# Performance work log

Measured on AMD Instinct MI355X. Metric: run time of the kernel, lower is better.

Reference implementation:

```python
import jax, jax.numpy as jnp
import numpy as np

N = 50000
E = 800000
IN_C = 512
HID = 256
OUT_C = 2
NUM_LAYERS = 3
NUM_HIER = 3
EPS = 1e-5


def setup_inputs() -> dict:
    key = jax.random.key(0)
    ks = jax.random.split(key, 24)
    g = lambda k, shp, fan: jax.random.normal(k, shp, jnp.float32) / np.sqrt(fan)
    inp = {
        "x": jax.random.normal(ks[0], (N, IN_C), jnp.float32),
        "edge_index": jax.random.randint(ks[1], (2, E), 0, N, jnp.int64),
        # GCN conv weights/biases
        "conv_w0": g(ks[2], (IN_C, HID), IN_C),
        "conv_ws": g(ks[3], (NUM_LAYERS - 1, HID, HID), HID),
        "conv_b": jnp.zeros((NUM_LAYERS, HID), jnp.float32),
        "bn_g": jnp.ones((NUM_LAYERS, HID), jnp.float32),
        "bn_b": jnp.zeros((NUM_LAYERS, HID), jnp.float32),
        # global-path MLPs
        "fcg_w0": g(ks[4], (HID, HID), HID),
        "fcg_ws": g(ks[5], (NUM_HIER - 1, 2 * HID, HID), 2 * HID),
        "fcg_b": jnp.zeros((NUM_HIER, HID), jnp.float32),
        "bng_g": jnp.ones((NUM_HIER, HID), jnp.float32),
        "bng_b": jnp.zeros((NUM_HIER, HID), jnp.float32),
        # local-path MLPs
        "fcl_w": g(ks[6], (NUM_HIER, HID, HID), HID),
        "fcl_b": jnp.zeros((NUM_HIER, HID), jnp.float32),
        "bnl_g": jnp.ones((NUM_HIER, HID), jnp.float32),
        "bnl_b": jnp.zeros((NUM_HIER, HID), jnp.float32),
        # output heads
        "outg_w": g(ks[7], (HID, OUT_C), HID),
        "outg_b": jnp.zeros((OUT_C,), jnp.float32),
        "outl_w": g(ks[8], (NUM_HIER, HID, OUT_C), HID),
        "outl_b": jnp.zeros((NUM_HIER, OUT_C), jnp.float32),
    }
    return inp


def _gcn_edges(edge_index):
    # add self-loops, compute symmetric normalization D^-1/2 (A+I) D^-1/2
    loops = jnp.arange(N, dtype=edge_index.dtype)
    rows = jnp.concatenate([edge_index[0], loops])
    cols = jnp.concatenate([edge_index[1], loops])
    deg = jax.ops.segment_sum(jnp.ones_like(rows, jnp.float32), rows, num_segments=N)
    dinv = jnp.where(deg > 0, jax.lax.rsqrt(deg), 0.0)
    w = dinv[rows] * dinv[cols]
    return rows, cols, w


def _propagate(h, rows, cols, w):
    msg = h[cols] * w[:, None]          # [E+N, HID] gather
    return jax.ops.segment_sum(msg, rows, num_segments=N)


def _bn(h, gamma, beta):
    m = h.mean(0)
    v = h.var(0)
    return gamma * (h - m) * jax.lax.rsqrt(v + EPS) + beta


def reference(x, edge_index, conv_w0, conv_ws, conv_b, bn_g, bn_b,
              fcg_w0, fcg_ws, fcg_b, bng_g, bng_b,
              fcl_w, fcl_b, bnl_g, bnl_b,
              outg_w, outg_b, outl_w, outl_b):
    rows, cols, ew = _gcn_edges(edge_index)
    h = x
    for i in range(NUM_LAYERS):
        W = conv_w0 if i == 0 else conv_ws[i - 1]
        h = _propagate(h @ W, rows, cols, ew) + conv_b[i]
        h = jax.nn.relu(_bn(h, bn_g[i], bn_b[i]))  # dropout = identity (eval)
    # hierarchical global path
    hg = []
    xg = jax.nn.relu(_bn(h @ fcg_w0 + fcg_b[0], bng_g[0], bng_b[0]))
    hg.append(xg)
    for i in range(NUM_HIER - 1):
        xg = jnp.concatenate([hg[i], h], -1) @ fcg_ws[i] + fcg_b[i + 1]
        xg = jax.nn.relu(_bn(xg, bng_g[i + 1], bng_b[i + 1]))
        hg.append(xg)
    og = jax.nn.log_softmax(hg[-1] @ outg_w + outg_b, axis=-1)
    # local heads
    ol = []
    for i in range(NUM_HIER):
        hl = jax.nn.relu(_bn(hg[i] @ fcl_w[i] + fcl_b[i], bnl_g[i], bnl_b[i]))
        ol.append(jax.nn.log_softmax(hl @ outl_w[i] + outl_b[i], axis=-1))
    # stack: [1 + NUM_HIER, N, OUT_C] (og first, then local heads)
    return jnp.stack([og] + ol, axis=0)
```

## Files before the change

kernel.cpp:

```cpp
#include <hip/hip_runtime.h>
#include <math.h>

#define N_NODES 50000
#define E_EDGES 800000
#define HID 256
#define EPS_BN 1e-5f

#define AGG_BPS 256

typedef __attribute__((ext_vector_type(8))) short short8;
typedef __attribute__((ext_vector_type(4))) float floatx4;
typedef __attribute__((ext_vector_type(8))) unsigned short ushort8v;

__device__ __forceinline__ unsigned short f2bf(float f) {
    unsigned u = __float_as_uint(f);
    u = (u + 0x7FFFu + ((u >> 16) & 1u)) >> 16;
    return (unsigned short)u;
}
__device__ __forceinline__ float bf2f(unsigned short b) {
    return __uint_as_float(((unsigned)b) << 16);
}
__device__ __forceinline__ void bn_scsh(const float* stats, const float* gamma,
                                        const float* beta, int ch,
                                        float& sc, float& sh) {
    const float invn = 1.0f / (float)N_NODES;
    float mean = stats[ch] * invn;
    float var = stats[HID + ch] * invn - mean * mean;
    var = fmaxf(var, 0.f);
    sc = gamma[ch] * rsqrtf(var + EPS_BN);
    sh = beta[ch] - mean * sc;
}

__global__ __launch_bounds__(256) void k_deg(const int* __restrict__ rows,
                                             int* __restrict__ deg) {
    int e = blockIdx.x * 256 + threadIdx.x;
    atomicAdd(&deg[rows[e]], 1);
}

__global__ __launch_bounds__(256) void k_dinv(const int* __restrict__ deg,
                                              float* __restrict__ dinv) {
    int n = blockIdx.x * 256 + threadIdx.x;
    if (n < N_NODES) dinv[n] = rsqrtf((float)deg[n] + 1.0f);
}

__global__ __launch_bounds__(1024) void k_scan(const int* __restrict__ deg,
                                               int* __restrict__ rowptr) {
    __shared__ int wsum[16];
    __shared__ int carry_s;
    int tid = threadIdx.x, lane = tid & 63, w = tid >> 6;
    if (tid == 0) carry_s = 0;
    __syncthreads();
    for (int base = 0; base < N_NODES; base += 1024) {
        int v = (base + tid < N_NODES) ? deg[base + tid] : 0;
        int x = v;
#pragma unroll
        for (int d = 1; d < 64; d <<= 1) {
            int t = __shfl_up(x, d);
            if (lane >= d) x += t;
        }
        if (lane == 63) wsum[w] = x;
        __syncthreads();
        if (w == 0) {
            int ws = (lane < 16) ? wsum[lane] : 0;
#pragma unroll
            for (int d = 1; d < 16; d <<= 1) {
                int t = __shfl_up(ws, d);
                if (lane >= d) ws += t;
            }
            if (lane < 16) wsum[lane] = ws;
        }
        __syncthreads();
        int c = carry_s;
        int wbase = (w > 0) ? wsum[w - 1] : 0;
        if (base + tid < N_NODES) rowptr[base + tid] = c + wbase + x - v;
        __syncthreads();
        if (tid == 0) carry_s = c + wsum[15];
        __syncthreads();
    }
    if (threadIdx.x == 0) rowptr[N_NODES] = carry_s;
}

__global__ __launch_bounds__(256) void k_fill(const int* __restrict__ rows,
                                              const int* __restrict__ cols,
                                              const int* __restrict__ rowptr,
                                              int* __restrict__ cursor,
                                              int* __restrict__ colidx) {
    int e = blockIdx.x * 256 + threadIdx.x;
    int r = rows[e];
    int pos = atomicAdd(&cursor[r], 1);
    colidx[rowptr[r] + pos] = cols[e];
}

__global__ __launch_bounds__(256) void k_f2bf_slice(const float* __restrict__ X,
                                                    unsigned short* __restrict__ Y) {
    int i = blockIdx.x * 256 + threadIdx.x;
    int slice = i / (N_NODES * 4);
    int rem = i - slice * (N_NODES * 4);
    int node = rem >> 2, p8 = rem & 3;
    const float* xp = X + (size_t)node * 512 + slice * 32 + p8 * 8;
    float4 va = ((const float4*)xp)[0];
    float4 vb = ((const float4*)xp)[1];
    ushort8v o;
    o[0] = f2bf(va.x); o[1] = f2bf(va.y); o[2] = f2bf(va.z); o[3] = f2bf(va.w);
    o[4] = f2bf(vb.x); o[5] = f2bf(vb.y); o[6] = f2bf(vb.z); o[7] = f2bf(vb.w);
    *(ushort8v*)(Y + (size_t)i * 8) = o;
}

__global__ __launch_bounds__(256) void k_wt(const float* __restrict__ W,
                                            unsigned short* __restrict__ Wt,
                                            int K) {
    int idx = blockIdx.x * 256 + threadIdx.x;
    if (idx >= K * HID) return;
    int k = idx >> 8;
    int n = idx & (HID - 1);
    Wt[(size_t)n * K + k] = f2bf(W[idx]);
}

__global__ __launch_bounds__(256) void k_gemm_mfma(
    const unsigned short* __restrict__ A0,
    const unsigned short* __restrict__ A1, int K0, int K,
    const unsigned short* __restrict__ Bt,
    unsigned short* __restrict__ C,
    const float* __restrict__ rowscale,
    float* __restrict__ stats)
{
    __shared__ alignas(16) unsigned short As[128 * 32];
    __shared__ alignas(16) unsigned short Bs[128 * 32];
    int tid = threadIdx.x;
    int wid = tid >> 6, lane = tid & 63;
    int row0 = blockIdx.x * 128;
    int n0 = blockIdx.y * 128;
    int wrow = (wid & 1) * 64, wcol = (wid >> 1) * 64;
    int lr = lane >> 2;
    int lk = (lane & 3) * 8;
    int qq = lane >> 4, mr = lane & 15;

    floatx4 acc[4][4];
#pragma unroll
    for (int i = 0; i < 4; ++i)
#pragma unroll
        for (int j = 0; j < 4; ++j) {
            floatx4 z = {0.f, 0.f, 0.f, 0.f};
            acc[i][j] = z;
        }

    for (int k0 = 0; k0 < K; k0 += 32) {
        const unsigned short* Abase =
            (k0 < K0) ? A0 + (size_t)(k0 >> 5) * (N_NODES * 32)
                      : A1 + (size_t)((k0 - K0) >> 5) * (N_NODES * 32);
#pragma unroll
        for (int i = 0; i < 2; ++i) {
            int rloc = wid * 32 + i * 16 + lr;
            int grow = row0 + rloc;
            if (grow > N_NODES - 1) grow = N_NODES - 1;
            const unsigned short* g = Abase + (size_t)grow * 32 + lk;
            unsigned short* l = As + (wid * 32 + i * 16) * 32;
            __builtin_amdgcn_global_load_lds(
                (const __attribute__((address_space(1))) void*)g,
                (__attribute__((address_space(3))) void*)l, 16, 0, 0);
        }
#pragma unroll
        for (int i = 0; i < 2; ++i) {
            int nloc = wid * 32 + i * 16 + lr;
            const unsigned short* g = Bt + (size_t)(n0 + nloc) * K + k0 + lk;
            unsigned short* l = Bs + (wid * 32 + i * 16) * 32;
            __builtin_amdgcn_global_load_lds(
                (const __attribute__((address_space(1))) void*)g,
                (__attribute__((address_space(3))) void*)l, 16, 0, 0);
        }
        __syncthreads();
        short8 af[4], bfv[4];
#pragma unroll
        for (int i = 0; i < 4; ++i)
            af[i] = *(const short8*)(As + (wrow + i * 16 + mr) * 32 + qq * 8);
#pragma unroll
        for (int j = 0; j < 4; ++j)
            bfv[j] = *(const short8*)(Bs + (wcol + j * 16 + mr) * 32 + qq * 8);
#pragma unroll
        for (int i = 0; i < 4; ++i)
#pragma unroll
            for (int j = 0; j < 4; ++j)
                acc[i][j] = __builtin_amdgcn_mfma_f32_16x16x32_bf16(
                    af[i], bfv[j], acc[i][j], 0, 0, 0);
        __syncthreads();
    }

    float* ls = (float*)As;
    float* lq = ((float*)As) + 128;
    if (stats) {
        ((float*)As)[tid] = 0.f;
        __syncthreads();
    }

    float psum[4] = {0.f, 0.f, 0.f, 0.f};
    float psq[4]  = {0.f, 0.f, 0.f, 0.f};
#pragma unroll
    for (int i = 0; i < 4; ++i) {
        int rbase = row0 + wrow + i * 16 + qq * 4;
#pragma unroll
        for (int r = 0; r < 4; ++r) {
            int row = rbase + r;
            if (row >= N_NODES) continue;
            float rs = rowscale ? rowscale[row] : 1.0f;
#pragma unroll
            for (int j = 0; j < 4; ++j) {
                int col = n0 + wcol + j * 16 + mr;
                float v = acc[i][j][r] * rs;
                C[((size_t)(col >> 5) * N_NODES + row) * 32 + (col & 31)] = f2bf(v);
                psum[j] += v;
                psq[j] += v * v;
            }
        }
    }
    if (stats) {
#pragma unroll
        for (int j = 0; j < 4; ++j) {
            int lc = wcol + j * 16 + mr;
            atomicAdd(&ls[lc], psum[j]);
            atomicAdd(&lq[lc], psq[j]);
        }
        __syncthreads();
        if (tid < 128) atomicAdd(&stats[n0 + tid], ls[tid]);
        else atomicAdd(&stats[HID + n0 + (tid - 128)], lq[tid - 128]);
    }
}

__global__ __launch_bounds__(256) void k_aggregate_bf(
    const unsigned short* __restrict__ g,
    unsigned short* __restrict__ outp,
    const int* __restrict__ rowptr,
    const int* __restrict__ colidx,
    const float* __restrict__ dinv,
    float* __restrict__ stats) {
    int lane = threadIdx.x & 63;
    int wid = threadIdx.x >> 6;
    int slice = blockIdx.x & 7;
    int bslice = blockIdx.x >> 3;
    const unsigned short* gs = g + (size_t)slice * (N_NODES * 32);
    unsigned short* os = outp + (size_t)slice * (N_NODES * 32);
    int g8 = lane >> 3;
    int l8 = lane & 7;
    int wavebase = (bslice * 4 + wid) * 8;
    const int stride = AGG_BPS * 4 * 8;

    float sa0 = 0.f, sa1 = 0.f, sa2 = 0.f, sa3 = 0.f;
    float qa0 = 0.f, qa1 = 0.f, qa2 = 0.f, qa3 = 0.f;

    for (int nb = wavebase; nb < N_NODES; nb += stride) {
        int node = nb + g8;
        bool valid = node < N_NODES;
        int nc = valid ? node : N_NODES - 1;
        int s = rowptr[nc];
        int e = valid ? rowptr[nc + 1] : s;
        int e1 = e - 1;
        auto cl = [&](int j) { int t = j < e1 ? j : e1; return t > 0 ? t : 0; };

        ushort4 sv = *(const ushort4*)(gs + ((size_t)nc << 5) + (l8 << 2));
        float rs = dinv[nc];
        float a0 = bf2f(sv.x), a1 = bf2f(sv.y), a2 = bf2f(sv.z), a3 = bf2f(sv.w);

        int cn0 = colidx[cl(s)], cn1 = colidx[cl(s + 1)];
        ushort4 vn0 = *(const ushort4*)(gs + ((size_t)cn0 << 5) + (l8 << 2));
        ushort4 vn1 = *(const ushort4*)(gs + ((size_t)cn1 << 5) + (l8 << 2));
        cn0 = colidx[cl(s + 2)];
        cn1 = colidx[cl(s + 3)];

        for (int i = s; i < e; i += 2) {
            ushort4 u0 = vn0, u1 = vn1;
            vn0 = *(const ushort4*)(gs + ((size_t)cn0 << 5) + (l8 << 2));
            vn1 = *(const ushort4*)(gs + ((size_t)cn1 << 5) + (l8 << 2));
            cn0 = colidx[cl(i + 4)];
            cn1 = colidx[cl(i + 5)];
            float m1 = (i + 1 < e) ? 1.f : 0.f;
            a0 += bf2f(u0.x); a1 += bf2f(u0.y);
            a2 += bf2f(u0.z); a3 += bf2f(u0.w);
            a0 = fmaf(m1, bf2f(u1.x), a0); a1 = fmaf(m1, bf2f(u1.y), a1);
            a2 = fmaf(m1, bf2f(u1.z), a2); a3 = fmaf(m1, bf2f(u1.w), a3);
        }
        if (valid) {
            float r0 = a0 * rs, r1 = a1 * rs, r2 = a2 * rs, r3 = a3 * rs;
            ushort4 o;
            o.x = f2bf(r0); o.y = f2bf(r1); o.z = f2bf(r2); o.w = f2bf(r3);
            union { ushort4 u4; unsigned long long u64; } cvt;
            cvt.u4 = o;
            __builtin_nontemporal_store(
                cvt.u64, (unsigned long long*)(os + ((size_t)node << 5) + (l8 << 2)));
            sa0 += r0; sa1 += r1; sa2 += r2; sa3 += r3;
            qa0 += r0 * r0; qa1 += r1 * r1; qa2 += r2 * r2; qa3 += r3 * r3;
        }
    }
#pragma unroll
    for (int off = 8; off < 64; off <<= 1) {
        sa0 += __shfl_xor(sa0, off); sa1 += __shfl_xor(sa1, off);
        sa2 += __shfl_xor(sa2, off); sa3 += __shfl_xor(sa3, off);
        qa0 += __shfl_xor(qa0, off); qa1 += __shfl_xor(qa1, off);
        qa2 += __shfl_xor(qa2, off); qa3 += __shfl_xor(qa3, off);
    }
    __shared__ float ls[32], lq[32];
    if (threadIdx.x < 32) { ls[threadIdx.x] = 0.f; lq[threadIdx.x] = 0.f; }
    __syncthreads();
    if (lane < 8) {
        atomicAdd(&ls[l8 * 4 + 0], sa0); atomicAdd(&lq[l8 * 4 + 0], qa0);
        atomicAdd(&ls[l8 * 4 + 1], sa1); atomicAdd(&lq[l8 * 4 + 1], qa1);
        atomicAdd(&ls[l8 * 4 + 2], sa2); atomicAdd(&lq[l8 * 4 + 2], qa2);
        atomicAdd(&ls[l8 * 4 + 3], sa3); atomicAdd(&lq[l8 * 4 + 3], qa3);
    }
    __syncthreads();
    if (threadIdx.x < 32) {
        atomicAdd(&stats[slice * 32 + threadIdx.x], ls[threadIdx.x]);
        atomicAdd(&stats[HID + slice * 32 + threadIdx.x], lq[threadIdx.x]);
    }
}

__global__ __launch_bounds__(256) void k_bnapply_bf(const unsigned short* __restrict__ X,
                                                    unsigned short* __restrict__ Y,
                                                    const float* __restrict__ stats,
                                                    const float* __restrict__ gamma,
                                                    const float* __restrict__ beta) {
    int i = blockIdx.x * 256 + threadIdx.x;
    int slice = i / (N_NODES * 4);
    int rem = i - slice * (N_NODES * 4);
    int ch8 = slice * 32 + (rem & 3) * 8;
    ushort8v v = *(const ushort8v*)(X + (size_t)i * 8);
    ushort8v o;
#pragma unroll
    for (int k = 0; k < 8; ++k) {
        float sc, sh;
        bn_scsh(stats, gamma, beta, ch8 + k, sc, sh);
        float f = bf2f((unsigned short)v[k]);
        o[k] = f2bf(fmaxf(f * sc + sh, 0.f));
    }
    *(ushort8v*)(Y + (size_t)i * 8) = o;
}

__global__ __launch_bounds__(256) void k_head_bf(const unsigned short* __restrict__ H,
                                                 const float* __restrict__ stats,
                                                 const float* __restrict__ gamma,
                                                 const float* __restrict__ beta,
                                                 const float* __restrict__ W,
                                                 const float* __restrict__ b,
                                                 float* __restrict__ outp) {
    int wave = (blockIdx.x * 256 + threadIdx.x) >> 6;
    int lane = threadIdx.x & 63;
    if (wave >= N_NODES) return;
    ushort4 h4 = *(const ushort4*)(
        H + ((size_t)(lane >> 3) * N_NODES + wave) * 32 + (lane & 7) * 4);
    float h0 = bf2f(h4.x), h1 = bf2f(h4.y), h2 = bf2f(h4.z), h3 = bf2f(h4.w);
    if (stats) {
        int ch = lane * 4;
        float sc, sh;
        bn_scsh(stats, gamma, beta, ch + 0, sc, sh); h0 = fmaxf(h0 * sc + sh, 0.f);
        bn_scsh(stats, gamma, beta, ch + 1, sc, sh); h1 = fmaxf(h1 * sc + sh, 0.f);
        bn_scsh(stats, gamma, beta, ch + 2, sc, sh); h2 = fmaxf(h2 * sc + sh, 0.f);
        bn_scsh(stats, gamma, beta, ch + 3, sc, sh); h3 = fmaxf(h3 * sc + sh, 0.f);
    }
    const float2* W2 = (const float2*)W;
    float2 w0 = W2[lane * 4 + 0], w1 = W2[lane * 4 + 1];
    float2 w2 = W2[lane * 4 + 2], w3 = W2[lane * 4 + 3];
    float p0 = h0 * w0.x + h1 * w1.x + h2 * w2.x + h3 * w3.x;
    float p1 = h0 * w0.y + h1 * w1.y + h2 * w2.y + h3 * w3.y;
    for (int off = 32; off > 0; off >>= 1) {
        p0 += __shfl_down(p0, off);
        p1 += __shfl_down(p1, off);
    }
    if (lane == 0) {
        float z0 = p0 + b[0], z1 = p1 + b[1];
        float m = fmaxf(z0, z1);
        float lse = m + logf(expf(z0 - m) + expf(z1 - m));
        outp[(size_t)wave * 2 + 0] = z0 - lse;
        outp[(size_t)wave * 2 + 1] = z1 - lse;
    }
}

extern "C" void kernel_launch(void* const* d_in, const int* in_sizes, int n_in,
                              void* d_out, int out_size, void* d_ws, size_t ws_size,
                              hipStream_t stream) {
    const float* x       = (const float*)d_in[0];
    const int*   ei      = (const int*)d_in[1];
    const float* conv_w0 = (const float*)d_in[2];
    const float* conv_ws = (const float*)d_in[3];
    const float* bn_g    = (const float*)d_in[5];
    const float* bn_b    = (const float*)d_in[6];
    const float* fcg_w0  = (const float*)d_in[7];
    const float* fcg_ws  = (const float*)d_in[8];
    const float* bng_g   = (const float*)d_in[10];
    const float* bng_b   = (const float*)d_in[11];
    const float* fcl_w   = (const float*)d_in[12];
    const float* bnl_g   = (const float*)d_in[14];
    const float* bnl_b   = (const float*)d_in[15];
    const float* outg_w  = (const float*)d_in[16];
    const float* outg_b  = (const float*)d_in[17];
    const float* outl_w  = (const float*)d_in[18];
    const float* outl_b  = (const float*)d_in[19];
    float* out = (float*)d_out;

    const int* rows = ei;
    const int* cols = ei + E_EDGES;

    char* ws = (char*)d_ws;
    size_t off = 0;
    auto carve = [&](size_t bytes) -> void* {
        void* p = ws + off;
        off = (off + bytes + 255) & ~(size_t)255;
        return p;
    };
    const size_t ACT = (size_t)N_NODES * HID * 2;
    unsigned short* xbf = (unsigned short*)carve((size_t)N_NODES * 512 * 2);
    unsigned short* tG  = (unsigned short*)carve(ACT);
    unsigned short* tA  = (unsigned short*)carve(ACT);
    unsigned short* hbf = (unsigned short*)carve(ACT);
    unsigned short* g1  = (unsigned short*)carve(ACT);
    unsigned short* g2  = (unsigned short*)carve(ACT);
    unsigned short* wt_conv0 = (unsigned short*)carve(256 * 512 * 2);
    unsigned short* wt_conv1 = (unsigned short*)carve(256 * 256 * 2);
    unsigned short* wt_conv2 = (unsigned short*)carve(256 * 256 * 2);
    unsigned short* wt_fcg0  = (unsigned short*)carve(256 * 256 * 2);
    unsigned short* wt_fcgs0 = (unsigned short*)carve(256 * 512 * 2);
    unsigned short* wt_fcgs1 = (unsigned short*)carve(256 * 512 * 2);
    unsigned short* wt_fcl0  = (unsigned short*)carve(256 * 256 * 2);
    unsigned short* wt_fcl1  = (unsigned short*)carve(256 * 256 * 2);
    unsigned short* wt_fcl2  = (unsigned short*)carve(256 * 256 * 2);
    int*   deg    = (int*)carve(2 * 50048 * 4);
    int*   cursor = deg + 50048;
    int*   rowptr = (int*)carve((size_t)(N_NODES + 1) * 4);
    float* dinv   = (float*)carve((size_t)N_NODES * 4);
    int*   colidx = (int*)carve((size_t)E_EDGES * 4);
    float* stats_all = (float*)carve(9 * 2 * HID * 4);
    (void)off; (void)ws_size; (void)in_sizes; (void)n_in; (void)out_size;

    hipMemsetAsync(deg, 0, 2 * 50048 * 4, stream);
    hipMemsetAsync(stats_all, 0, 9 * 2 * HID * 4, stream);
    k_deg<<<E_EDGES / 256, 256, 0, stream>>>(rows, deg);
    k_dinv<<<(N_NODES + 255) / 256, 256, 0, stream>>>(deg, dinv);
    k_scan<<<1, 1024, 0, stream>>>(deg, rowptr);
    k_fill<<<E_EDGES / 256, 256, 0, stream>>>(rows, cols, rowptr, cursor, colidx);

    k_f2bf_slice<<<N_NODES * 64 / 256, 256, 0, stream>>>(x, xbf);
    k_wt<<<(512 * 256 + 255) / 256, 256, 0, stream>>>(conv_w0, wt_conv0, 512);
    k_wt<<<(256 * 256 + 255) / 256, 256, 0, stream>>>(conv_ws, wt_conv1, 256);
    k_wt<<<(256 * 256 + 255) / 256, 256, 0, stream>>>(conv_ws + 65536, wt_conv2, 256);
    k_wt<<<(256 * 256 + 255) / 256, 256, 0, stream>>>(fcg_w0, wt_fcg0, 256);
    k_wt<<<(512 * 256 + 255) / 256, 256, 0, stream>>>(fcg_ws, wt_fcgs0, 512);
    k_wt<<<(512 * 256 + 255) / 256, 256, 0, stream>>>(fcg_ws + 131072, wt_fcgs1, 512);
    k_wt<<<(256 * 256 + 255) / 256, 256, 0, stream>>>(fcl_w, wt_fcl0, 256);
    k_wt<<<(256 * 256 + 255) / 256, 256, 0, stream>>>(fcl_w + 65536, wt_fcl1, 256);
    k_wt<<<(256 * 256 + 255) / 256, 256, 0, stream>>>(fcl_w + 131072, wt_fcl2, 256);

    dim3 ggrid((N_NODES + 127) / 128, 2);
    auto gemm = [&](const unsigned short* A0, const unsigned short* A1,
                    int K0, int K, const unsigned short* Bt, unsigned short* C,
                    const float* rs, float* st) {
        k_gemm_mfma<<<ggrid, 256, 0, stream>>>(A0, A1, K0, K, Bt, C, rs, st);
    };
    auto bnapply = [&](float* st, const unsigned short* X, unsigned short* Y,
                       const float* gamma, const float* beta) {
        k_bnapply_bf<<<N_NODES * 32 / 256, 256, 0, stream>>>(X, Y, st, gamma, beta);
    };
    auto agg = [&](const unsigned short* in, unsigned short* outb, float* st) {
        k_aggregate_bf<<<8 * AGG_BPS, 256, 0, stream>>>(in, outb, rowptr, colidx,
                                                        dinv, st);
    };
    float* st;

    st = stats_all + 0 * 512;
    gemm(xbf, nullptr, 512, 512, wt_conv0, tG, dinv, nullptr);
    agg(tG, tA, st);
    bnapply(st, tA, g1, bn_g + 0, bn_b + 0);
    st = stats_all + 1 * 512;
    gemm(g1, nullptr, 256, 256, wt_conv1, tG, dinv, nullptr);
    agg(tG, tA, st);
    bnapply(st, tA, g2, bn_g + 256, bn_b + 256);
    st = stats_all + 2 * 512;
    gemm(g2, nullptr, 256, 256, wt_conv2, tG, dinv, nullptr);
    agg(tG, tA, st);
    bnapply(st, tA, hbf, bn_g + 512, bn_b + 512);

    st = stats_all + 3 * 512;
    gemm(hbf, nullptr, 256, 256, wt_fcg0, tG, nullptr, st);
    bnapply(st, tG, g1, bng_g + 0, bng_b + 0);
    st = stats_all + 4 * 512;
    gemm(g1, nullptr, 256, 256, wt_fcl0, tG, nullptr, st);
    k_head_bf<<<N_NODES / 4, 256, 0, stream>>>(tG, st, bnl_g + 0, bnl_b + 0,
                                               outl_w, outl_b,
                                               out + (size_t)1 * N_NODES * 2);
    st = stats_all + 5 * 512;
    gemm(g1, hbf, 256, 512, wt_fcgs0, tG, nullptr, st);
    bnapply(st, tG, g2, bng_g + 256, bng_b + 256);
    st = stats_all + 6 * 512;
    gemm(g2, nullptr, 256, 256, wt_fcl1, tG, nullptr, st);
    k_head_bf<<<N_NODES / 4, 256, 0, stream>>>(tG, st, bnl_g + 256, bnl_b + 256,
                                               outl_w + 512, outl_b + 2,
                                               out + (size_t)2 * N_NODES * 2);
    st = stats_all + 7 * 512;
    gemm(g2, hbf, 256, 512, wt_fcgs1, tG, nullptr, st);
    bnapply(st, tG, g1, bng_g + 512, bng_b + 512);
    st = stats_all + 8 * 512;
    gemm(g1, nullptr, 256, 256, wt_fcl2, tG, nullptr, st);
    k_head_bf<<<N_NODES / 4, 256, 0, stream>>>(tG, st, bnl_g + 512, bnl_b + 512,
                                               outl_w + 1024, outl_b + 4,
                                               out + (size_t)3 * N_NODES * 2);
    k_head_bf<<<N_NODES / 4, 256, 0, stream>>>(g1, nullptr, nullptr, nullptr,
                                               outg_w, outg_b, out);
}
```

Measured before the change: 1.019 ms.

## Parallelize row-pointer scan, widen GEMM K-step, and vectorize aggregation loads

Replaces the single-block serial scan over node degrees with a three-kernel multi-block scan (per-chunk scan, block-sum scan, offset add). The MFMA GEMM now loads two 32-wide K slices per barrier pair, which halves the number of syncs per K. The aggregation kernel has each lane handle 8 channels with 16-byte loads instead of 4, and prefetches neighbors deeper. Together these aim to cut the serial scan latency, the GEMM barrier overhead and the gather instruction count, at the cost of more LDS, more registers and two extra launches.

```diff
diff --git a/kernel.cpp b/kernel.cpp
--- a/kernel.cpp
+++ b/kernel.cpp
@@ -7,6 +7,9 @@
 #define EPS_BN 1e-5f
 
 #define AGG_BPS 256
+
+#define SCAN_CHUNK 1024
+#define SCAN_NCH ((N_NODES + SCAN_CHUNK - 1) / SCAN_CHUNK)
 
 typedef __attribute__((ext_vector_type(8))) short short8;
 typedef __attribute__((ext_vector_type(4))) float floatx4;
@@ -43,41 +46,53 @@
     if (n < N_NODES) dinv[n] = rsqrtf((float)deg[n] + 1.0f);
 }
 
-__global__ __launch_bounds__(1024) void k_scan(const int* __restrict__ deg,
-                                               int* __restrict__ rowptr) {
+__global__ __launch_bounds__(1024) void k_scan1(const int* __restrict__ deg,
+                                                int* __restrict__ rowptr,
+                                                int* __restrict__ bsum) {
     __shared__ int wsum[16];
-    __shared__ int carry_s;
     int tid = threadIdx.x, lane = tid & 63, w = tid >> 6;
-    if (tid == 0) carry_s = 0;
+    int idx = blockIdx.x * SCAN_CHUNK + tid;
+    int v = (idx < N_NODES) ? deg[idx] : 0;
+    int x = v;
+#pragma unroll
+    for (int d = 1; d < 64; d <<= 1) {
+        int t = __shfl_up(x, d);
+        if (lane >= d) x += t;
+    }
+    if (lane == 63) wsum[w] = x;
     __syncthreads();
-    for (int base = 0; base < N_NODES; base += 1024) {
-        int v = (base + tid < N_NODES) ? deg[base + tid] : 0;
-        int x = v;
-#pragma unroll
-        for (int d = 1; d < 64; d <<= 1) {
-            int t = __shfl_up(x, d);
-            if (lane >= d) x += t;
-        }
-        if (lane == 63) wsum[w] = x;
-        __syncthreads();
-        if (w == 0) {
-            int ws = (lane < 16) ? wsum[lane] : 0;
-#pragma unroll
-            for (int d = 1; d < 16; d <<= 1) {
-                int t = __shfl_up(ws, d);
-                if (lane >= d) ws += t;
-            }
-            if (lane < 16) wsum[lane] = ws;
-        }
-        __syncthreads();
-        int c = carry_s;
-        int wbase = (w > 0) ? wsum[w - 1] : 0;
-        if (base + tid < N_NODES) rowptr[base + tid] = c + wbase + x - v;
-        __syncthreads();
-        if (tid == 0) carry_s = c + wsum[15];
-        __syncthreads();
-    }
-    if (threadIdx.x == 0) rowptr[N_NODES] = carry_s;
+    if (w == 0) {
+        int ws = (lane < 16) ? wsum[lane] : 0;
+#pragma unroll
+        for (int d = 1; d < 16; d <<= 1) {
+            int t = __shfl_up(ws, d);
+            if (lane >= d) ws += t;
+        }
+        if (lane < 16) wsum[lane] = ws;
+    }
+    __syncthreads();
+    int wbase = (w > 0) ? wsum[w - 1] : 0;
+    if (idx < N_NODES) rowptr[idx] = wbase + x - v;
+    if (tid == 0) bsum[blockIdx.x] = wsum[15];
+}
+__global__ __launch_bounds__(64) void k_scan2(const int* __restrict__ bsum,
+                                              int* __restrict__ boff) {
+    int lane = threadIdx.x;
+    int v = (lane < SCAN_NCH) ? bsum[lane] : 0;
+    int x = v;
+#pragma unroll
+    for (int d = 1; d < 64; d <<= 1) {
+        int t = __shfl_up(x, d);
+        if (lane >= d) x += t;
+    }
+    if (lane < SCAN_NCH) boff[lane] = x - v;
+    if (lane == SCAN_NCH - 1) boff[SCAN_NCH] = x;
+}
+__global__ __launch_bounds__(1024) void k_scan3(int* __restrict__ rowptr,
+                                                const int* __restrict__ boff) {
+    int idx = blockIdx.x * SCAN_CHUNK + threadIdx.x;
+    if (idx < N_NODES) rowptr[idx] += boff[blockIdx.x];
+    if (blockIdx.x == 0 && threadIdx.x == 0) rowptr[N_NODES] = boff[SCAN_NCH];
 }
 
 __global__ __launch_bounds__(256) void k_fill(const int* __restrict__ rows,
@@ -124,8 +139,8 @@
     const float* __restrict__ rowscale,
     float* __restrict__ stats)
 {
-    __shared__ alignas(16) unsigned short As[128 * 32];
-    __shared__ alignas(16) unsigned short Bs[128 * 32];
+    __shared__ alignas(16) unsigned short As[2][128 * 32];
+    __shared__ alignas(16) unsigned short Bs[2][128 * 32];
     int tid = threadIdx.x;
     int wid = tid >> 6, lane = tid & 63;
     int row0 = blockIdx.x * 128;
@@ -144,44 +159,51 @@
             acc[i][j] = z;
         }
 
-    for (int k0 = 0; k0 < K; k0 += 32) {
-        const unsigned short* Abase =
-            (k0 < K0) ? A0 + (size_t)(k0 >> 5) * (N_NODES * 32)
-                      : A1 + (size_t)((k0 - K0) >> 5) * (N_NODES * 32);
-#pragma unroll
-        for (int i = 0; i < 2; ++i) {
-            int rloc = wid * 32 + i * 16 + lr;
-            int grow = row0 + rloc;
-            if (grow > N_NODES - 1) grow = N_NODES - 1;
-            const unsigned short* g = Abase + (size_t)grow * 32 + lk;
-            unsigned short* l = As + (wid * 32 + i * 16) * 32;
-            __builtin_amdgcn_global_load_lds(
-                (const __attribute__((address_space(1))) void*)g,
-                (__attribute__((address_space(3))) void*)l, 16, 0, 0);
-        }
-#pragma unroll
-        for (int i = 0; i < 2; ++i) {
-            int nloc = wid * 32 + i * 16 + lr;
-            const unsigned short* g = Bt + (size_t)(n0 + nloc) * K + k0 + lk;
-            unsigned short* l = Bs + (wid * 32 + i * 16) * 32;
-            __builtin_amdgcn_global_load_lds(
-                (const __attribute__((address_space(1))) void*)g,
-                (__attribute__((address_space(3))) void*)l, 16, 0, 0);
+    for (int k0 = 0; k0 < K; k0 += 64) {
+#pragma unroll
+        for (int h = 0; h < 2; ++h) {
+            int kk = k0 + h * 32;
+            const unsigned short* Abase =
+                (kk < K0) ? A0 + (size_t)(kk >> 5) * (N_NODES * 32)
+                          : A1 + (size_t)((kk - K0) >> 5) * (N_NODES * 32);
+#pragma unroll
+            for (int i = 0; i < 2; ++i) {
+                int rloc = wid * 32 + i * 16 + lr;
+                int grow = row0 + rloc;
+                if (grow > N_NODES - 1) grow = N_NODES - 1;
+                const unsigned short* gp = Abase + (size_t)grow * 32 + lk;
+                unsigned short* l = As[h] + (wid * 32 + i * 16) * 32;
+                __builtin_amdgcn_global_load_lds(
+                    (const __attribute__((address_space(1))) void*)gp,
+                    (__attribute__((address_space(3))) void*)l, 16, 0, 0);
+            }
+#pragma unroll
+            for (int i = 0; i < 2; ++i) {
+                int nloc = wid * 32 + i * 16 + lr;
+                const unsigned short* gp = Bt + (size_t)(n0 + nloc) * K + kk + lk;
+                unsigned short* l = Bs[h] + (wid * 32 + i * 16) * 32;
+                __builtin_amdgcn_global_load_lds(
+                    (const __attribute__((address_space(1))) void*)gp,
+                    (__attribute__((address_space(3))) void*)l, 16, 0, 0);
+            }
         }
         __syncthreads();
-        short8 af[4], bfv[4];
-#pragma unroll
-        for (int i = 0; i < 4; ++i)
-            af[i] = *(const short8*)(As + (wrow + i * 16 + mr) * 32 + qq * 8);
-#pragma unroll
-        for (int j = 0; j < 4; ++j)
-            bfv[j] = *(const short8*)(Bs + (wcol + j * 16 + mr) * 32 + qq * 8);
-#pragma unroll
-        for (int i = 0; i < 4; ++i)
+#pragma unroll
+        for (int h = 0; h < 2; ++h) {
+            short8 af[4], bfv[4];
+#pragma unroll
+            for (int i = 0; i < 4; ++i)
+                af[i] = *(const short8*)(As[h] + (wrow + i * 16 + mr) * 32 + qq * 8);
 #pragma unroll
             for (int j = 0; j < 4; ++j)
-                acc[i][j] = __builtin_amdgcn_mfma_f32_16x16x32_bf16(
-                    af[i], bfv[j], acc[i][j], 0, 0, 0);
+                bfv[j] = *(const short8*)(Bs[h] + (wcol + j * 16 + mr) * 32 + qq * 8);
+#pragma unroll
+            for (int i = 0; i < 4; ++i)
+#pragma unroll
+                for (int j = 0; j < 4; ++j)
+                    acc[i][j] = __builtin_amdgcn_mfma_f32_16x16x32_bf16(
+                        af[i], bfv[j], acc[i][j], 0, 0, 0);
+        }
         __syncthreads();
     }
 
@@ -238,16 +260,17 @@
     int bslice = blockIdx.x >> 3;
     const unsigned short* gs = g + (size_t)slice * (N_NODES * 32);
     unsigned short* os = outp + (size_t)slice * (N_NODES * 32);
-    int g8 = lane >> 3;
-    int l8 = lane & 7;
-    int wavebase = (bslice * 4 + wid) * 8;
-    const int stride = AGG_BPS * 4 * 8;
-
-    float sa0 = 0.f, sa1 = 0.f, sa2 = 0.f, sa3 = 0.f;
-    float qa0 = 0.f, qa1 = 0.f, qa2 = 0.f, qa3 = 0.f;
+    int g4 = lane >> 2;
+    int l4 = lane & 3;
+    int wavebase = (bslice * 4 + wid) * 16;
+    const int stride = AGG_BPS * 4 * 16;
+
+    float sa[8], qa[8];
+#pragma unroll
+    for (int k = 0; k < 8; ++k) { sa[k] = 0.f; qa[k] = 0.f; }
 
     for (int nb = wavebase; nb < N_NODES; nb += stride) {
-        int node = nb + g8;
+        int node = nb + g4;
         bool valid = node < N_NODES;
         int nc = valid ? node : N_NODES - 1;
         int s = rowptr[nc];
@@ -255,55 +278,64 @@
         int e1 = e - 1;
         auto cl = [&](int j) { int t = j < e1 ? j : e1; return t > 0 ? t : 0; };
 
-        ushort4 sv = *(const ushort4*)(gs + ((size_t)nc << 5) + (l8 << 2));
+        ushort8v sv = *(const ushort8v*)(gs + ((size_t)nc << 5) + (l4 << 3));
         float rs = dinv[nc];
-        float a0 = bf2f(sv.x), a1 = bf2f(sv.y), a2 = bf2f(sv.z), a3 = bf2f(sv.w);
-
-        int cn0 = colidx[cl(s)], cn1 = colidx[cl(s + 1)];
-        ushort4 vn0 = *(const ushort4*)(gs + ((size_t)cn0 << 5) + (l8 << 2));
-        ushort4 vn1 = *(const ushort4*)(gs + ((size_t)cn1 << 5) + (l8 << 2));
-        cn0 = colidx[cl(s + 2)];
-        cn1 = colidx[cl(s + 3)];
+        float a[8];
+#pragma unroll
+        for (int k = 0; k < 8; ++k) a[k] = bf2f((unsigned short)sv[k]);
+
+        int c00 = colidx[cl(s)],     c01 = colidx[cl(s + 1)];
+        int c10 = colidx[cl(s + 2)], c11 = colidx[cl(s + 3)];
+        ushort8v v00 = *(const ushort8v*)(gs + ((size_t)c00 << 5) + (l4 << 3));
+        ushort8v v01 = *(const ushort8v*)(gs + ((size_t)c01 << 5) + (l4 << 3));
+        ushort8v v10 = *(const ushort8v*)(gs + ((size_t)c10 << 5) + (l4 << 3));
+        ushort8v v11 = *(const ushort8v*)(gs + ((size_t)c11 << 5) + (l4 << 3));
+        int c20 = colidx[cl(s + 4)], c21 = colidx[cl(s + 5)];
 
         for (int i = s; i < e; i += 2) {
-            ushort4 u0 = vn0, u1 = vn1;
-            vn0 = *(const ushort4*)(gs + ((size_t)cn0 << 5) + (l8 << 2));
-            vn1 = *(const ushort4*)(gs + ((size_t)cn1 << 5) + (l8 << 2));
-            cn0 = colidx[cl(i + 4)];
-            cn1 = colidx[cl(i + 5)];
+            ushort8v u0 = v00, u1 = v01;
+            v00 = v10; v01 = v11;
+            v10 = *(const ushort8v*)(gs + ((size_t)c20 << 5) + (l4 << 3));
+            v11 = *(const ushort8v*)(gs + ((size_t)c21 << 5) + (l4 << 3));
+            c20 = colidx[cl(i + 6)];
+            c21 = colidx[cl(i + 7)];
             float m1 = (i + 1 < e) ? 1.f : 0.f;
-            a0 += bf2f(u0.x); a1 += bf2f(u0.y);
-            a2 += bf2f(u0.z); a3 += bf2f(u0.w);
-            a0 = fmaf(m1, bf2f(u1.x), a0); a1 = fmaf(m1, bf2f(u1.y), a1);
-            a2 = fmaf(m1, bf2f(u1.z), a2); a3 = fmaf(m1, bf2f(u1.w), a3);
+#pragma unroll
+            for (int k = 0; k < 8; ++k) {
+                a[k] += bf2f((unsigned short)u0[k]);
+                a[k] = fmaf(m1, bf2f((unsigned short)u1[k]), a[k]);
+            }
         }
         if (valid) {
-            float r0 = a0 * rs, r1 = a1 * rs, r2 = a2 * rs, r3 = a3 * rs;
-            ushort4 o;
-            o.x = f2bf(r0); o.y = f2bf(r1); o.z = f2bf(r2); o.w = f2bf(r3);
-            union { ushort4 u4; unsigned long long u64; } cvt;
-            cvt.u4 = o;
+            ushort8v o;
+#pragma unroll
+            for (int k = 0; k < 8; ++k) {
+                float r = a[k] * rs;
+                o[k] = f2bf(r);
+                sa[k] += r;
+                qa[k] += r * r;
+            }
             __builtin_nontemporal_store(
-                cvt.u64, (unsigned long long*)(os + ((size_t)node << 5) + (l8 << 2)));
-            sa0 += r0; sa1 += r1; sa2 += r2; sa3 += r3;
-            qa0 += r0 * r0; qa1 += r1 * r1; qa2 += r2 * r2; qa3 += r3 * r3;
-        }
-    }
-#pragma unroll
-    for (int off = 8; off < 64; off <<= 1) {
-        sa0 += __shfl_xor(sa0, off); sa1 += __shfl_xor(sa1, off);
-        sa2 += __shfl_xor(sa2, off); sa3 += __shfl_xor(sa3, off);
-        qa0 += __shfl_xor(qa0, off); qa1 += __shfl_xor(qa1, off);
-        qa2 += __shfl_xor(qa2, off); qa3 += __shfl_xor(qa3, off);
+                o, (ushort8v*)(os + ((size_t)node << 5) + (l4 << 3)));
+        }
+    }
+#pragma unroll
+    for (int off = 4; off < 64; off <<= 1) {
+#pragma unroll
+        for (int k = 0; k < 8; ++k) {
+            sa[k] += __shfl_xor(sa[k], off);
+            qa[k] += __shfl_xor(qa[k], off);
+        }
     }
     __shared__ float ls[32], lq[32];
     if (threadIdx.x < 32) { ls[threadIdx.x] = 0.f; lq[threadIdx.x] = 0.f; }
     __syncthreads();
-    if (lane < 8) {
-        atomicAdd(&ls[l8 * 4 + 0], sa0); atomicAdd(&lq[l8 * 4 + 0], qa0);
-        atomicAdd(&ls[l8 * 4 + 1], sa1); atomicAdd(&lq[l8 * 4 + 1], qa1);
-        atomicAdd(&ls[l8 * 4 + 2], sa2); atomicAdd(&lq[l8 * 4 + 2], qa2);
-        atomicAdd(&ls[l8 * 4 + 3], sa3); atomicAdd(&lq[l8 * 4 + 3], qa3);
+    if (lane < 4) {
+#pragma unroll
+        for (int k = 0; k < 8; ++k) {
+            atomicAdd(&ls[lane * 8 + k], sa[k]);
+            atomicAdd(&lq[lane * 8 + k], qa[k]);
+        }
     }
     __syncthreads();
     if (threadIdx.x < 32) {
@@ -426,13 +458,18 @@
     float* dinv   = (float*)carve((size_t)N_NODES * 4);
     int*   colidx = (int*)carve((size_t)E_EDGES * 4);
     float* stats_all = (float*)carve(9 * 2 * HID * 4);
+    int*   scanbuf = (int*)carve(512);
+    int*   bsum = scanbuf;
+    int*   boff = scanbuf + 64;
     (void)off; (void)ws_size; (void)in_sizes; (void)n_in; (void)out_size;
 
     hipMemsetAsync(deg, 0, 2 * 50048 * 4, stream);
     hipMemsetAsync(stats_all, 0, 9 * 2 * HID * 4, stream);
     k_deg<<<E_EDGES / 256, 256, 0, stream>>>(rows, deg);
     k_dinv<<<(N_NODES + 255) / 256, 256, 0, stream>>>(deg, dinv);
-    k_scan<<<1, 1024, 0, stream>>>(deg, rowptr);
+    k_scan1<<<SCAN_NCH, 1024, 0, stream>>>(deg, rowptr, bsum);
+    k_scan2<<<1, 64, 0, stream>>>(bsum, boff);
+    k_scan3<<<SCAN_NCH, 1024, 0, stream>>>(rowptr, boff);
     k_fill<<<E_EDGES / 256, 256, 0, stream>>>(rows, cols, rowptr, cursor, colidx);
 
     k_f2bf_slice<<<N_NODES * 64 / 256, 256, 0, stream>>>(x, xbf);
```

New measurement: 983.2 us. 1.04x faster.

## Parallelize scan, batch weight transposes, stage GEMM output in LDS, cache BN params

Applied to the files above, without the earlier changes.

Several independent changes. The single-block serial prefix scan becomes a three-kernel block scan. Per-matrix weight transpose launches are merged into batched launches. The GEMM now loads two 32-wide K slices per barrier, and its epilogue stages the bf16 output tile in padded LDS so it can be written to global memory with coalesced 16-byte stores. The BN-apply and output-head kernels compute scale and shift once per block into shared memory instead of per element. Together these target launch overhead, a serialized scan, scattered 2-byte global stores and redundant rsqrt work, at the cost of more LDS per GEMM block, which may lower occupancy.

```diff
diff --git a/kernel.cpp b/kernel.cpp
--- a/kernel.cpp
+++ b/kernel.cpp
@@ -7,6 +7,9 @@
 #define EPS_BN 1e-5f
 
 #define AGG_BPS 256
+
+#define SCAN_CHUNK 1024
+#define SCAN_NCH ((N_NODES + SCAN_CHUNK - 1) / SCAN_CHUNK)
 
 typedef __attribute__((ext_vector_type(8))) short short8;
 typedef __attribute__((ext_vector_type(4))) float floatx4;
@@ -43,41 +46,53 @@
     if (n < N_NODES) dinv[n] = rsqrtf((float)deg[n] + 1.0f);
 }
 
-__global__ __launch_bounds__(1024) void k_scan(const int* __restrict__ deg,
-                                               int* __restrict__ rowptr) {
+__global__ __launch_bounds__(1024) void k_scan1(const int* __restrict__ deg,
+                                                int* __restrict__ rowptr,
+                                                int* __restrict__ bsum) {
     __shared__ int wsum[16];
-    __shared__ int carry_s;
     int tid = threadIdx.x, lane = tid & 63, w = tid >> 6;
-    if (tid == 0) carry_s = 0;
-    __syncthreads();
-    for (int base = 0; base < N_NODES; base += 1024) {
-        int v = (base + tid < N_NODES) ? deg[base + tid] : 0;
-        int x = v;
-#pragma unroll
-        for (int d = 1; d < 64; d <<= 1) {
-            int t = __shfl_up(x, d);
-            if (lane >= d) x += t;
-        }
-        if (lane == 63) wsum[w] = x;
-        __syncthreads();
-        if (w == 0) {
-            int ws = (lane < 16) ? wsum[lane] : 0;
-#pragma unroll
-            for (int d = 1; d < 16; d <<= 1) {
-                int t = __shfl_up(ws, d);
-                if (lane >= d) ws += t;
-            }
-            if (lane < 16) wsum[lane] = ws;
-        }
-        __syncthreads();
-        int c = carry_s;
-        int wbase = (w > 0) ? wsum[w - 1] : 0;
-        if (base + tid < N_NODES) rowptr[base + tid] = c + wbase + x - v;
-        __syncthreads();
-        if (tid == 0) carry_s = c + wsum[15];
-        __syncthreads();
-    }
-    if (threadIdx.x == 0) rowptr[N_NODES] = carry_s;
+    int idx = blockIdx.x * SCAN_CHUNK + tid;
+    int v = (idx < N_NODES) ? deg[idx] : 0;
+    int x = v;
+#pragma unroll
+    for (int d = 1; d < 64; d <<= 1) {
+        int t = __shfl_up(x, d);
+        if (lane >= d) x += t;
+    }
+    if (lane == 63) wsum[w] = x;
+    __syncthreads();
+    if (w == 0) {
+        int ws = (lane < 16) ? wsum[lane] : 0;
+#pragma unroll
+        for (int d = 1; d < 16; d <<= 1) {
+            int t = __shfl_up(ws, d);
+            if (lane >= d) ws += t;
+        }
+        if (lane < 16) wsum[lane] = ws;
+    }
+    __syncthreads();
+    int wbase = (w > 0) ? wsum[w - 1] : 0;
+    if (idx < N_NODES) rowptr[idx] = wbase + x - v;
+    if (tid == 0) bsum[blockIdx.x] = wsum[15];
+}
+__global__ __launch_bounds__(64) void k_scan2(const int* __restrict__ bsum,
+                                              int* __restrict__ boff) {
+    int lane = threadIdx.x;
+    int v = (lane < SCAN_NCH) ? bsum[lane] : 0;
+    int x = v;
+#pragma unroll
+    for (int d = 1; d < 64; d <<= 1) {
+        int t = __shfl_up(x, d);
+        if (lane >= d) x += t;
+    }
+    if (lane < SCAN_NCH) boff[lane] = x - v;
+    if (lane == SCAN_NCH - 1) boff[SCAN_NCH] = x;
+}
+__global__ __launch_bounds__(1024) void k_scan3(int* __restrict__ rowptr,
+                                                const int* __restrict__ boff) {
+    int idx = blockIdx.x * SCAN_CHUNK + threadIdx.x;
+    if (idx < N_NODES) rowptr[idx] += boff[blockIdx.x];
+    if (blockIdx.x == 0 && threadIdx.x == 0) rowptr[N_NODES] = boff[SCAN_NCH];
 }
 
 __global__ __launch_bounds__(256) void k_fill(const int* __restrict__ rows,
@@ -108,12 +123,15 @@
 
 __global__ __launch_bounds__(256) void k_wt(const float* __restrict__ W,
                                             unsigned short* __restrict__ Wt,
-                                            int K) {
+                                            int K, int total) {
     int idx = blockIdx.x * 256 + threadIdx.x;
-    if (idx >= K * HID) return;
-    int k = idx >> 8;
-    int n = idx & (HID - 1);
-    Wt[(size_t)n * K + k] = f2bf(W[idx]);
+    if (idx >= total) return;
+    int KS = K << 8;
+    int m = idx / KS;
+    int rel = idx - m * KS;
+    int k = rel >> 8;
+    int n = rel & 255;
+    Wt[(size_t)m * KS + (size_t)n * K + k] = f2bf(W[idx]);
 }
 
 __global__ __launch_bounds__(256) void k_gemm_mfma(
@@ -124,8 +142,9 @@
     const float* __restrict__ rowscale,
     float* __restrict__ stats)
 {
-    __shared__ alignas(16) unsigned short As[128 * 32];
-    __shared__ alignas(16) unsigned short Bs[128 * 32];
+    __shared__ alignas(16) unsigned char smem[36864];
+    unsigned short* AsB = (unsigned short*)smem;
+    unsigned short* BsB = (unsigned short*)(smem + 16384);
     int tid = threadIdx.x;
     int wid = tid >> 6, lane = tid & 63;
     int row0 = blockIdx.x * 128;
@@ -144,74 +163,80 @@
             acc[i][j] = z;
         }
 
-    for (int k0 = 0; k0 < K; k0 += 32) {
-        const unsigned short* Abase =
-            (k0 < K0) ? A0 + (size_t)(k0 >> 5) * (N_NODES * 32)
-                      : A1 + (size_t)((k0 - K0) >> 5) * (N_NODES * 32);
-#pragma unroll
-        for (int i = 0; i < 2; ++i) {
-            int rloc = wid * 32 + i * 16 + lr;
-            int grow = row0 + rloc;
-            if (grow > N_NODES - 1) grow = N_NODES - 1;
-            const unsigned short* g = Abase + (size_t)grow * 32 + lk;
-            unsigned short* l = As + (wid * 32 + i * 16) * 32;
-            __builtin_amdgcn_global_load_lds(
-                (const __attribute__((address_space(1))) void*)g,
-                (__attribute__((address_space(3))) void*)l, 16, 0, 0);
-        }
-#pragma unroll
-        for (int i = 0; i < 2; ++i) {
-            int nloc = wid * 32 + i * 16 + lr;
-            const unsigned short* g = Bt + (size_t)(n0 + nloc) * K + k0 + lk;
-            unsigned short* l = Bs + (wid * 32 + i * 16) * 32;
-            __builtin_amdgcn_global_load_lds(
-                (const __attribute__((address_space(1))) void*)g,
-                (__attribute__((address_space(3))) void*)l, 16, 0, 0);
+    for (int k0 = 0; k0 < K; k0 += 64) {
+#pragma unroll
+        for (int h = 0; h < 2; ++h) {
+            int kk = k0 + h * 32;
+            const unsigned short* Abase =
+                (kk < K0) ? A0 + (size_t)(kk >> 5) * (N_NODES * 32)
+                          : A1 + (size_t)((kk - K0) >> 5) * (N_NODES * 32);
+#pragma unroll
+            for (int i = 0; i < 2; ++i) {
+                int rloc = wid * 32 + i * 16 + lr;
+                int grow = row0 + rloc;
+                if (grow > N_NODES - 1) grow = N_NODES - 1;
+                const unsigned short* gp = Abase + (size_t)grow * 32 + lk;
+                unsigned short* l = AsB + h * 4096 + (wid * 32 + i * 16) * 32;
+                __builtin_amdgcn_global_load_lds(
+                    (const __attribute__((address_space(1))) void*)gp,
+                    (__attribute__((address_space(3))) void*)l, 16, 0, 0);
+            }
+#pragma unroll
+            for (int i = 0; i < 2; ++i) {
+                int nloc = wid * 32 + i * 16 + lr;
+                const unsigned short* gp = Bt + (size_t)(n0 + nloc) * K + kk + lk;
+                unsigned short* l = BsB + h * 4096 + (wid * 32 + i * 16) * 32;
+                __builtin_amdgcn_global_load_lds(
+                    (const __attribute__((address_space(1))) void*)gp,
+                    (__attribute__((address_space(3))) void*)l, 16, 0, 0);
+            }
         }
         __syncthreads();
-        short8 af[4], bfv[4];
-#pragma unroll
-        for (int i = 0; i < 4; ++i)
-            af[i] = *(const short8*)(As + (wrow + i * 16 + mr) * 32 + qq * 8);
-#pragma unroll
-        for (int j = 0; j < 4; ++j)
-            bfv[j] = *(const short8*)(Bs + (wcol + j * 16 + mr) * 32 + qq * 8);
-#pragma unroll
-        for (int i = 0; i < 4; ++i)
+#pragma unroll
+        for (int h = 0; h < 2; ++h) {
+            short8 af[4], bfv[4];
+#pragma unroll
+            for (int i = 0; i < 4; ++i)
+                af[i] = *(const short8*)(AsB + h * 4096 + (wrow + i * 16 + mr) * 32 + qq * 8);
 #pragma unroll
             for (int j = 0; j < 4; ++j)
-                acc[i][j] = __builtin_amdgcn_mfma_f32_16x16x32_bf16(
-                    af[i], bfv[j], acc[i][j], 0, 0, 0);
+                bfv[j] = *(const short8*)(BsB + h * 4096 + (wcol + j * 16 + mr) * 32 + qq * 8);
+#pragma unroll
+            for (int i = 0; i < 4; ++i)
+#pragma unroll
+                for (int j = 0; j < 4; ++j)
+                    acc[i][j] = __builtin_amdgcn_mfma_f32_16x16x32_bf16(
+                        af[i], bfv[j], acc[i][j], 0, 0, 0);
+        }
         __syncthreads();
     }
 
-    float* ls = (float*)As;
-    float* lq = ((float*)As) + 128;
-    if (stats) {
-        ((float*)As)[tid] = 0.f;
-        __syncthreads();
-    }
+    unsigned short* lds_c = (unsigned short*)smem;
+    float* ls = (float*)(smem + 34816);
+    float* lq = ls + 128;
+    if (stats) ((float*)(smem + 34816))[tid] = 0.f;
 
     float psum[4] = {0.f, 0.f, 0.f, 0.f};
     float psq[4]  = {0.f, 0.f, 0.f, 0.f};
 #pragma unroll
     for (int i = 0; i < 4; ++i) {
-        int rbase = row0 + wrow + i * 16 + qq * 4;
+        int trow_base = wrow + i * 16 + qq * 4;
 #pragma unroll
         for (int r = 0; r < 4; ++r) {
-            int row = rbase + r;
-            if (row >= N_NODES) continue;
-            float rs = rowscale ? rowscale[row] : 1.0f;
+            int trow = trow_base + r;
+            int grow = row0 + trow;
+            bool rok = grow < N_NODES;
+            float rs = 1.0f;
+            if (rowscale && rok) rs = rowscale[grow];
 #pragma unroll
             for (int j = 0; j < 4; ++j) {
-                int col = n0 + wcol + j * 16 + mr;
                 float v = acc[i][j][r] * rs;
-                C[((size_t)(col >> 5) * N_NODES + row) * 32 + (col & 31)] = f2bf(v);
-                psum[j] += v;
-                psq[j] += v * v;
+                lds_c[trow * 136 + wcol + j * 16 + mr] = f2bf(v);
+                if (rok) { psum[j] += v; psq[j] += v * v; }
             }
         }
     }
+    __syncthreads();
     if (stats) {
 #pragma unroll
         for (int j = 0; j < 4; ++j) {
@@ -219,6 +244,21 @@
             atomicAdd(&ls[lc], psum[j]);
             atomicAdd(&lq[lc], psq[j]);
         }
+    }
+    int rowlim = N_NODES - row0; if (rowlim > 128) rowlim = 128;
+    int sbase = n0 >> 5;
+#pragma unroll
+    for (int u = 0; u < 8; ++u) {
+        int uid = tid + 256 * u;
+        int row = uid >> 4;
+        int q = (uid >> 2) & 3;
+        int sub = uid & 3;
+        if (row < rowlim) {
+            ushort8v vv = *(const ushort8v*)(lds_c + row * 136 + q * 32 + sub * 8);
+            *(ushort8v*)(C + ((size_t)(sbase + q) * N_NODES + row0 + row) * 32 + sub * 8) = vv;
+        }
+    }
+    if (stats) {
         __syncthreads();
         if (tid < 128) atomicAdd(&stats[n0 + tid], ls[tid]);
         else atomicAdd(&stats[HID + n0 + (tid - 128)], lq[tid - 128]);
@@ -317,18 +357,28 @@
                                                     const float* __restrict__ stats,
                                                     const float* __restrict__ gamma,
                                                     const float* __restrict__ beta) {
+    __shared__ float s_sc[64], s_sh[64];
     int i = blockIdx.x * 256 + threadIdx.x;
+    int slice_lo = (blockIdx.x * 256) / (N_NODES * 4);
+    int slice_hi = (blockIdx.x * 256 + 255) / (N_NODES * 4);
+    if (threadIdx.x < 64) {
+        int half = threadIdx.x >> 5;
+        int c = threadIdx.x & 31;
+        int sl = half ? slice_hi : slice_lo;
+        float sc, sh;
+        bn_scsh(stats, gamma, beta, sl * 32 + c, sc, sh);
+        s_sc[threadIdx.x] = sc; s_sh[threadIdx.x] = sh;
+    }
+    __syncthreads();
     int slice = i / (N_NODES * 4);
-    int rem = i - slice * (N_NODES * 4);
-    int ch8 = slice * 32 + (rem & 3) * 8;
+    int sel = (slice != slice_lo) ? 32 : 0;
+    int c8 = sel + (i & 3) * 8;
     ushort8v v = *(const ushort8v*)(X + (size_t)i * 8);
     ushort8v o;
 #pragma unroll
     for (int k = 0; k < 8; ++k) {
-        float sc, sh;
-        bn_scsh(stats, gamma, beta, ch8 + k, sc, sh);
         float f = bf2f((unsigned short)v[k]);
-        o[k] = f2bf(fmaxf(f * sc + sh, 0.f));
+        o[k] = f2bf(fmaxf(f * s_sc[c8 + k] + s_sh[c8 + k], 0.f));
     }
     *(ushort8v*)(Y + (size_t)i * 8) = o;
 }
@@ -340,6 +390,13 @@
                                                  const float* __restrict__ W,
                                                  const float* __restrict__ b,
                                                  float* __restrict__ outp) {
+    __shared__ float h_sc[HID], h_sh[HID];
+    if (stats) {
+        float sc, sh;
+        bn_scsh(stats, gamma, beta, threadIdx.x, sc, sh);
+        h_sc[threadIdx.x] = sc; h_sh[threadIdx.x] = sh;
+    }
+    __syncthreads();
     int wave = (blockIdx.x * 256 + threadIdx.x) >> 6;
     int lane = threadIdx.x & 63;
     if (wave >= N_NODES) return;
@@ -348,11 +405,10 @@
     float h0 = bf2f(h4.x), h1 = bf2f(h4.y), h2 = bf2f(h4.z), h3 = bf2f(h4.w);
     if (stats) {
         int ch = lane * 4;
-        float sc, sh;
-        bn_scsh(stats, gamma, beta, ch + 0, sc, sh); h0 = fmaxf(h0 * sc + sh, 0.f);
-        bn_scsh(stats, gamma, beta, ch + 1, sc, sh); h1 = fmaxf(h1 * sc + sh, 0.f);
-        bn_scsh(stats, gamma, beta, ch + 2, sc, sh); h2 = fmaxf(h2 * sc + sh, 0.f);
-        bn_scsh(stats, gamma, beta, ch + 3, sc, sh); h3 = fmaxf(h3 * sc + sh, 0.f);
+        h0 = fmaxf(h0 * h_sc[ch + 0] + h_sh[ch + 0], 0.f);
+        h1 = fmaxf(h1 * h_sc[ch + 1] + h_sh[ch + 1], 0.f);
+        h2 = fmaxf(h2 * h_sc[ch + 2] + h_sh[ch + 2], 0.f);
+        h3 = fmaxf(h3 * h_sc[ch + 3] + h_sh[ch + 3], 0.f);
     }
     const float2* W2 = (const float2*)W;
     float2 w0 = W2[lane * 4 + 0], w1 = W2[lane * 4 + 1];
@@ -426,25 +482,26 @@
     float* dinv   = (float*)carve((size_t)N_NODES * 4);
     int*   colidx = (int*)carve((size_t)E_EDGES * 4);
     float* stats_all = (float*)carve(9 * 2 * HID * 4);
+    int*   scanbuf = (int*)carve(512);
+    int*   bsum = scanbuf;
+    int*   boff = scanbuf + 64;
     (void)off; (void)ws_size; (void)in_sizes; (void)n_in; (void)out_size;
 
     hipMemsetAsync(deg, 0, 2 * 50048 * 4, stream);
     hipMemsetAsync(stats_all, 0, 9 * 2 * HID * 4, stream);
     k_deg<<<E_EDGES / 256, 256, 0, stream>>>(rows, deg);
     k_dinv<<<(N_NODES + 255) / 256, 256, 0, stream>>>(deg, dinv);
-    k_scan<<<1, 1024, 0, stream>>>(deg, rowptr);
+    k_scan1<<<SCAN_NCH, 1024, 0, stream>>>(deg, rowptr, bsum);
+    k_scan2<<<1, 64, 0, stream>>>(bsum, boff);
+    k_scan3<<<SCAN_NCH, 1024, 0, stream>>>(rowptr, boff);
     k_fill<<<E_EDGES / 256, 256, 0, stream>>>(rows, cols, rowptr, cursor, colidx);
 
     k_f2bf_slice<<<N_NODES * 64 / 256, 256, 0, stream>>>(x, xbf);
-    k_wt<<<(512 * 256 + 255) / 256, 256, 0, stream>>>(conv_w0, wt_conv0, 512);
-    k_wt<<<(256 * 256 + 255) / 256, 256, 0, stream>>>(conv_ws, wt_conv1, 256);
-    k_wt<<<(256 * 256 + 255) / 256, 256, 0, stream>>>(conv_ws + 65536, wt_conv2, 256);
-    k_wt<<<(256 * 256 + 255) / 256, 256, 0, stream>>>(fcg_w0, wt_fcg0, 256);
-    k_wt<<<(512 * 256 + 255) / 256, 256, 0, stream>>>(fcg_ws, wt_fcgs0, 512);
-    k_wt<<<(512 * 256 + 255) / 256, 256, 0, stream>>>(fcg_ws + 131072, wt_fcgs1, 512);
-    k_wt<<<(256 * 256 + 255) / 256, 256, 0, stream>>>(fcl_w, wt_fcl0, 256);
-    k_wt<<<(256 * 256 + 255) / 256, 256, 0, stream>>>(fcl_w + 65536, wt_fcl1, 256);
-    k_wt<<<(256 * 256 + 255) / 256, 256, 0, stream>>>(fcl_w + 131072, wt_fcl2, 256);
+    k_wt<<<(512 * 256 + 255) / 256, 256, 0, stream>>>(conv_w0, wt_conv0, 512, 512 * 256);
+    k_wt<<<(2 * 256 * 256 + 255) / 256, 256, 0, stream>>>(conv_ws, wt_conv1, 256, 2 * 256 * 256);
+    k_wt<<<(256 * 256 + 255) / 256, 256, 0, stream>>>(fcg_w0, wt_fcg0, 256, 256 * 256);
+    k_wt<<<(2 * 512 * 256 + 255) / 256, 256, 0, stream>>>(fcg_ws, wt_fcgs0, 512, 2 * 512 * 256);
+    k_wt<<<(3 * 256 * 256 + 255) / 256, 256, 0, stream>>>(fcl_w, wt_fcl0, 256, 3 * 256 * 256);
 
     dim3 ggrid((N_NODES + 127) / 128, 2);
     auto gemm = [&](const unsigned short* A0, const unsigned short* A1,
```

Measured after the change: 928.3 us. 8.9% less time.
